# Kernel optimization log

Hardware: AMD Instinct MI355X
Metric: run time of the kernel (lower is better)

## Reference

```python
import jax, jax.numpy as jnp
import numpy as np

H, E, V = 1024, 8, 32000
B, S = 2, 2048
RANK, ALPHA = 4, 1.0
LORA_SCALE = ALPHA / RANK
TOP_K = 2
C1, DEC = 4096, 256
CACHE_SIZES = np.array([C1 - i * DEC for i in range(E)])  # [4096,...,2304]
CMAX = int(CACHE_SIZES.max())
H2 = H // 2  # pyramid compression ratio 0.5


def setup_inputs() -> dict:
    key = jax.random.key(0)
    ks = jax.random.split(key, 24)
    n = lambda k, shape, s=1.0: jax.random.normal(k, shape, dtype=jnp.float32) * s
    w = 1.0 / np.sqrt(H)
    inp = {
        "x": n(ks[0], (B, S, H)),
        "query": n(ks[1], (B, S, H)),
        "cache_values": n(ks[2], (E, CMAX, H)),
        "cache_importance": jax.random.uniform(ks[3], (E, CMAX), dtype=jnp.float32),
        "Wr": n(ks[4], (H, E), w),
        "Wexp": n(ks[5], (E, H, H), w),
        "bexp": jnp.zeros((E, H), jnp.float32),
        "Aexp": n(ks[6], (E, H, RANK), w),
        "Bexp": n(ks[7], (E, RANK, H), w),
        "Wq": n(ks[8], (H, H), w),
        "bq": jnp.zeros((H,), jnp.float32),
        "Wk": n(ks[9], (H, H), w),
        "bk": jnp.zeros((H,), jnp.float32),
        "Aq": n(ks[10], (H, RANK), w),
        "Bq": n(ks[11], (RANK, H), w),
        "Ak": n(ks[12], (H, RANK), w),
        "Bk": n(ks[13], (RANK, H), w),
        "Wd": n(ks[14], (H, H2), w),
        "Wu": n(ks[15], (H2, H), 1.0 / np.sqrt(H2)),
        "Av": n(ks[16], (E, H, RANK), w),
        "Bv": n(ks[17], (E, RANK, H), w),
        "Wv": n(ks[18], (H, V), w),
        "bv": jnp.zeros((V,), jnp.float32),
    }
    # compressor weights are per-expert in the original (one per KVCache)
    inp["Wd"] = n(ks[19], (E, H, H2), w)
    inp["Wu"] = n(ks[20], (E, H2, H), 1.0 / np.sqrt(H2))
    return inp


def reference(x, query, cache_values, cache_importance, Wr, Wexp, bexp, Aexp, Bexp,
              Wq, bq, Wk, bk, Aq, Bq, Ak, Bk, Wd, Wu, Av, Bv, Wv, bv):
    # ---- AdaptiveRouter: softmax gate, top-2, renormalize, scatter to dense ----
    gate = jax.nn.softmax(jnp.einsum("bsh,he->bse", x, Wr), axis=-1)       # [B,S,E]
    topv, topi = jax.lax.top_k(gate, TOP_K)                                 # [B,S,K]
    topv = topv / jnp.sum(topv, axis=-1, keepdims=True)
    rw = jnp.sum(jax.nn.one_hot(topi, E, dtype=x.dtype) * topv[..., None], axis=-2)  # [B,S,E]

    # ---- compute_token_importance: LoRA-augmented q/k projections + attention ----
    q = query @ Wq + bq + LORA_SCALE * ((query @ Aq) @ Bq)                  # [B,S,H]
    k = x @ Wk + bk + LORA_SCALE * ((x @ Ak) @ Bk)                          # [B,S,H]
    att = jax.nn.softmax(jnp.einsum("bqh,bkh->bqk", q, k) / np.sqrt(H), axis=-1)
    importance = jnp.sum(att, axis=1)                                       # [B,S] (sum over queries)

    # ---- per-expert KV cache: pyramid compress (down-gelu-up, importance gate) + value LoRA, masked mean ----
    valid = jnp.asarray(np.arange(CMAX)[None, :] < CACHE_SIZES[:, None], x.dtype)  # [E,Cmax]
    h = jax.nn.gelu(jnp.einsum("ech,ehd->ecd", cache_values, Wd))           # [E,Cmax,H2]
    comp = jnp.einsum("ecd,edh->ech", h, Wu) * jax.nn.sigmoid(cache_importance)[..., None]
    comp = comp + LORA_SCALE * jnp.einsum("ech,ehr,erd->ecd", comp, Av, Bv)
    cached = jnp.sum(comp * valid[..., None], axis=1) / jnp.asarray(CACHE_SIZES, x.dtype)[:, None]  # [E,H]

    # ---- dense loop over all LoRA experts (original runs every expert on every token) ----
    eo = jnp.einsum("bsh,ehd->bsed", x, Wexp) + bexp                        # [B,S,E,H]
    eo = eo + LORA_SCALE * jnp.einsum("bsh,ehr,erd->bsed", x, Aexp, Bexp)
    eo = eo + cached[None, None]                                            # broadcast cached values
    expert_output = jnp.einsum("bsed,bse->bsd", eo, rw)                     # routed combine

    logits = expert_output @ Wv + bv                                        # [B,S,V]
    return logits, importance
```

## Files before the change

### kernel.cpp

```cpp
#include <hip/hip_runtime.h>

typedef __bf16 bf16_t;
typedef __bf16 bf16x4 __attribute__((ext_vector_type(4)));
typedef __bf16 bf16x8 __attribute__((ext_vector_type(8)));
typedef float f32x4 __attribute__((ext_vector_type(4)));

#define AS1 __attribute__((address_space(1)))
#define AS3 __attribute__((address_space(3)))
#define BAR() asm volatile("s_barrier" ::: "memory")

__device__ __forceinline__ void gload_lds16(const void* g, void* l) {
  __builtin_amdgcn_global_load_lds((AS1 void*)g, (AS3 void*)l, 16, 0, 0);
}

__device__ __forceinline__ void stage_tile(const bf16_t* g, int ld, bf16_t* lds, int tid) {
  int w = tid >> 6, lane = tid & 63;
#pragma unroll
  for (int r = 0; r < 2; ++r) {
    int rowbase = r * 64 + w * 16;
    const bf16_t* gp = g + (long)(rowbase + (lane >> 2)) * ld + (lane & 3) * 8;
    bf16_t* lp = lds + rowbase * 32;
    gload_lds16(gp, lp);
  }
}

__device__ __forceinline__ void gemm_core(const bf16_t* A, const bf16_t* Bt, int lda, int ldb,
                                          int K, int rowBase, int colBase,
                                          bf16_t* As, bf16_t* Bs, f32x4 acc[4][4]) {
  int tid = threadIdx.x;
  int lane = tid & 63, w = tid >> 6;
  int wr = w >> 1, wc = w & 1;
  int lr = lane & 15, kg = lane >> 4;
  const bf16_t* Ab = A + (long)rowBase * lda;
  const bf16_t* Bb = Bt + (long)colBase * ldb;
  for (int kt = 0; kt < K; kt += 32) {
    __syncthreads();
    stage_tile(Ab + kt, lda, As, tid);
    stage_tile(Bb + kt, ldb, Bs, tid);
    __syncthreads();
    bf16x8 a[4], b[4];
#pragma unroll
    for (int m = 0; m < 4; ++m)
      a[m] = *(const bf16x8*)&As[(wr * 64 + m * 16 + lr) * 32 + kg * 8];
#pragma unroll
    for (int n = 0; n < 4; ++n)
      b[n] = *(const bf16x8*)&Bs[(wc * 64 + n * 16 + lr) * 32 + kg * 8];
#pragma unroll
    for (int m = 0; m < 4; ++m)
#pragma unroll
      for (int n = 0; n < 4; ++n)
        acc[m][n] = __builtin_amdgcn_mfma_f32_16x16x32_bf16(a[m], b[n], acc[m][n], 0, 0, 0);
  }
}

__device__ __forceinline__ void zero_acc(f32x4 acc[4][4]) {
#pragma unroll
  for (int m = 0; m < 4; ++m)
#pragma unroll
    for (int n = 0; n < 4; ++n)
#pragma unroll
      for (int i = 0; i < 4; ++i) acc[m][n][i] = 0.f;
}

__global__ __launch_bounds__(256) void k_cast(const float* in, bf16_t* out, long n4) {
  long i = (long)blockIdx.x * 256 + threadIdx.x;
  if (i >= n4) return;
  float4 v = ((const float4*)in)[i];
  bf16_t* o = out + i * 4;
  o[0] = (bf16_t)v.x; o[1] = (bf16_t)v.y; o[2] = (bf16_t)v.z; o[3] = (bf16_t)v.w;
}

__global__ __launch_bounds__(256) void k_prep_wt(const float* W, const float* A, const float* Bm,
                                                 bf16_t* out, int K, int N,
                                                 long wstride, long astride, long bstride, long ostride) {
  __shared__ float tile[64][65];
  int e = blockIdx.z;
  W += (long)e * wstride;
  out += (long)e * ostride;
  if (A) { A += (long)e * astride; Bm += (long)e * bstride; }
  int k0 = blockIdx.x * 64, n0 = blockIdx.y * 64;
  int tid = threadIdx.x;
  int tn = tid & 63, tk = tid >> 6;
#pragma unroll 4
  for (int i = 0; i < 16; ++i) {
    int k = tk + i * 4;
    float v = W[(long)(k0 + k) * N + (n0 + tn)];
    if (A) {
      const float* Ak = A + (long)(k0 + k) * 4;
      const float* Bn = Bm + n0 + tn;
      v += 0.25f * (Ak[0] * Bn[0] + Ak[1] * Bn[(long)N] + Ak[2] * Bn[2L * N] + Ak[3] * Bn[3L * N]);
    }
    tile[k][tn] = v;
  }
  __syncthreads();
#pragma unroll 4
  for (int i = 0; i < 16; ++i) {
    int n = tk + i * 4;
    out[(long)(n0 + n) * K + (k0 + tn)] = (bf16_t)tile[tn][n];
  }
}

__global__ __launch_bounds__(256) void k_router(const float* x, const float* Wr, float* rw) {
  int w = threadIdx.x >> 6, lane = threadIdx.x & 63;
  long tok = (long)blockIdx.x * 4 + w;
  const float* xr = x + tok * 1024;
  float acc[8] = {0.f, 0.f, 0.f, 0.f, 0.f, 0.f, 0.f, 0.f};
  for (int h = lane; h < 1024; h += 64) {
    float xv = xr[h];
    const float* wr8 = Wr + h * 8;
#pragma unroll
    for (int e = 0; e < 8; ++e) acc[e] += xv * wr8[e];
  }
#pragma unroll
  for (int o = 32; o; o >>= 1)
#pragma unroll
    for (int e = 0; e < 8; ++e) acc[e] += __shfl_xor(acc[e], o);
  if (lane == 0) {
    int i1 = 0;
    for (int e = 1; e < 8; ++e) if (acc[e] > acc[i1]) i1 = e;
    int i2 = (i1 == 0) ? 1 : 0;
    for (int e = 0; e < 8; ++e) { if (e == i1) continue; if (acc[e] > acc[i2]) i2 = e; }
    float g2 = expf(acc[i2] - acc[i1]);
    float d = 1.f / (1.f + g2);
    float* dst = rw + tok * 8;
#pragma unroll
    for (int e = 0; e < 8; ++e) dst[e] = (e == i1) ? d : ((e == i2) ? g2 * d : 0.f);
  }
}

__global__ __launch_bounds__(256) void k_gemm_bias_bf16(const bf16_t* A, const bf16_t* Bt,
                                                        const float* bias, bf16_t* out,
                                                        int K, int lda, int ldb, int ldc) {
  __shared__ bf16_t As[4096] __attribute__((aligned(16)));
  __shared__ bf16_t Bs[4096] __attribute__((aligned(16)));
  int rowBase = blockIdx.x * 128, colBase = blockIdx.y * 128;
  f32x4 acc[4][4];
  zero_acc(acc);
  gemm_core(A, Bt, lda, ldb, K, rowBase, colBase, As, Bs, acc);
  int tid = threadIdx.x, lane = tid & 63, w = tid >> 6;
  int wr = w >> 1, wc = w & 1, lc = lane & 15, kg = lane >> 4;
#pragma unroll
  for (int m = 0; m < 4; ++m)
#pragma unroll
    for (int n = 0; n < 4; ++n)
#pragma unroll
      for (int r = 0; r < 4; ++r) {
        int gr = rowBase + wr * 64 + m * 16 + kg * 4 + r;
        int gc = colBase + wc * 64 + n * 16 + lc;
        out[(long)gr * ldc + gc] = (bf16_t)(acc[m][n][r] + bias[gc]);
      }
}

template <bool NT>
__global__ __launch_bounds__(256) void k_gemm128(
    const bf16_t* __restrict__ A, long Az, const bf16_t* __restrict__ Bt, long Bz,
    const float* __restrict__ bias, float* __restrict__ out, long Oz,
    int mB, int N, int K, float scale) {
  __shared__ bf16_t As[4096] __attribute__((aligned(16)));
  __shared__ bf16_t Bs[4096] __attribute__((aligned(16)));
  __shared__ float fl[32 * 132];
  int tid = threadIdx.x;
  A += (long)blockIdx.y * Az;
  Bt += (long)blockIdx.y * Bz;
  out += (long)blockIdx.y * Oz;
  int per = gridDim.x >> 3;
  int bid = blockIdx.x;
  int swz = (bid & 7) * per + (bid >> 3);
  int rowB = swz % mB, colB = swz / mB;
  int rowBase = rowB << 7, colBase = colB << 7;
  f32x4 acc[4][4];
  zero_acc(acc);
  gemm_core(A, Bt, K, K, K, rowBase, colBase, As, Bs, acc);
  int lane = tid & 63, w = tid >> 6;
  int wr = w >> 1, wc = w & 1, lc = lane & 15, kg = lane >> 4;
  int colq = (tid & 31) * 4;
  f32x4 bb = {0.f, 0.f, 0.f, 0.f};
  if (bias) bb = *(const f32x4*)(bias + colBase + colq);
#pragma unroll
  for (int c = 0; c < 4; ++c) {
    __syncthreads();
    if (wr == (c >> 1)) {
      int m0 = (c & 1) * 2;
#pragma unroll
      for (int mm = 0; mm < 2; ++mm)
#pragma unroll
        for (int n = 0; n < 4; ++n)
#pragma unroll
          for (int r = 0; r < 4; ++r)
            fl[(mm * 16 + kg * 4 + r) * 132 + wc * 64 + n * 16 + lc] = acc[m0 + mm][n][r] * scale;
    }
    __syncthreads();
    long grow = rowBase + c * 32;
#pragma unroll
    for (int q = 0; q < 4; ++q) {
      int idx = q * 256 + tid;
      int row = idx >> 5;
      f32x4 v = *(const f32x4*)&fl[row * 132 + colq];
      v += bb;
      float* op = out + (grow + row) * (long)N + colBase + colq;
      if (NT) __builtin_nontemporal_store(v, (f32x4*)op);
      else *(f32x4*)op = v;
    }
  }
}

template <bool NT>
__global__ __launch_bounds__(512, 2) void k_gemm256(
    const bf16_t* __restrict__ A, long Az, const bf16_t* __restrict__ Bt, long Bz,
    const float* __restrict__ bias, float* __restrict__ out, long Oz,
    int mBlocks, int N, int K, int ntk, float scale) {
  __shared__ bf16_t lds[81920] __attribute__((aligned(16)));
  int tid = threadIdx.x;
  int lane = tid & 63, w = tid >> 6;
  int wr = w >> 2, wc = w & 3;
  int lr = lane & 15, kg = lane >> 4;
  A += (long)blockIdx.y * Az;
  Bt += (long)blockIdx.y * Bz;
  out += (long)blockIdx.y * Oz;

  int per = gridDim.x >> 3;
  int bid = blockIdx.x;
  int swz = (bid & 7) * per + (bid >> 3);
  int rowB = swz % mBlocks, colB = swz / mBlocks;
  long rowBase = (long)rowB << 8, colBase = (long)colB << 8;

  int colE = ((lane & 7) ^ (lane >> 3)) * 8;
  int r0 = w * 16 + (lane >> 3);
  const bf16_t* Ag = A + rowBase * K;
  const bf16_t* Bg = Bt + colBase * K;

  auto stageA = [&](int t, int h) {
    const bf16_t* g = Ag + (long)(h * 128 + r0) * K + t * 64 + colE;
    bf16_t* l = lds + (t & 1) * 16384 + h * 8192 + w * 1024;
    gload_lds16(g, l);
    gload_lds16(g + (long)8 * K, l + 512);
  };
  auto stageB = [&](int t, int h) {
    const bf16_t* g = Bg + (long)(h * 128 + r0) * K + t * 64 + colE;
    bf16_t* l = lds + 32768 + (t % 3) * 16384 + h * 8192 + w * 1024;
    gload_lds16(g, l);
    gload_lds16(g + (long)8 * K, l + 512);
  };

  f32x4 acc[8][4];
#pragma unroll
  for (int m = 0; m < 8; ++m)
#pragma unroll
    for (int n = 0; n < 4; ++n)
#pragma unroll
      for (int i = 0; i < 4; ++i) acc[m][n][i] = 0.f;

  stageB(0, 0); stageB(0, 1); stageA(0, 0); stageA(0, 1);
  if (ntk > 1) { stageB(1, 0); stageB(1, 1); }
  if (ntk > 1) asm volatile("s_waitcnt vmcnt(4)" ::: "memory");
  else         asm volatile("s_waitcnt vmcnt(0)" ::: "memory");
  BAR();

  for (int t = 0; t < ntk; ++t) {
    const bf16_t* Ar = lds + (t & 1) * 16384 + wr * 8192;
    const bf16_t* Br = lds + 32768 + (t % 3) * 16384 + (wc >> 1) * 8192;
    int bRowOff = (wc & 1) * 64;
    bf16x8 bfr[4][2];
#pragma unroll
    for (int p = 0; p < 4; ++p) {
      if (p == 0) {
#pragma unroll
        for (int n = 0; n < 4; ++n) {
          int R = bRowOff + n * 16 + lr;
#pragma unroll
          for (int ks = 0; ks < 2; ++ks)
            bfr[n][ks] = *(const bf16x8*)(Br + R * 64 + ((ks * 4 + kg) ^ (R & 7)) * 8);
        }
      }
      bf16x8 afr[2][2];
#pragma unroll
      for (int mm = 0; mm < 2; ++mm) {
        int R = p * 32 + mm * 16 + lr;
#pragma unroll
        for (int ks = 0; ks < 2; ++ks)
          afr[mm][ks] = *(const bf16x8*)(Ar + R * 64 + ((ks * 4 + kg) ^ (R & 7)) * 8);
      }
      if (p < 2) { if (t + 1 < ntk) stageA(t + 1, p); }
      else       { if (t + 2 < ntk) stageB(t + 2, p - 2); }
      BAR();
      asm volatile("s_waitcnt lgkmcnt(0)" ::: "memory");
      __builtin_amdgcn_sched_barrier(0);
      __builtin_amdgcn_s_setprio(1);
#pragma unroll
      for (int mm = 0; mm < 2; ++mm)
#pragma unroll
        for (int n = 0; n < 4; ++n)
#pragma unroll
          for (int ks = 0; ks < 2; ++ks)
            acc[p * 2 + mm][n] =
                __builtin_amdgcn_mfma_f32_16x16x32_bf16(afr[mm][ks], bfr[n][ks],
                                                        acc[p * 2 + mm][n], 0, 0, 0);
      __builtin_amdgcn_s_setprio(0);
      if (p == 3) {
        if (t + 2 < ntk)      asm volatile("s_waitcnt vmcnt(4)" ::: "memory");
        else if (t + 1 < ntk) asm volatile("s_waitcnt vmcnt(0)" ::: "memory");
      }
      BAR();
    }
  }

  float* fl = (float*)lds;
  f32x4 bb4 = {0.f, 0.f, 0.f, 0.f};
  if (bias) bb4 = ((const f32x4*)(bias + colBase))[lane];
#pragma unroll
  for (int c = 0; c < 4; ++c) {
    if ((c >> 1) == wr) {
      int mg0 = (c & 1) * 4;
#pragma unroll
      for (int j = 0; j < 4; ++j)
#pragma unroll
        for (int n = 0; n < 4; ++n) {
          int col = wc * 64 + n * 16 + lr;
          int lrow = j * 16 + kg * 4;
#pragma unroll
          for (int rr = 0; rr < 4; ++rr)
            fl[(lrow + rr) * 260 + col] = acc[mg0 + j][n][rr] * scale;
        }
    }
    BAR();
    long grow = rowBase + c * 64;
#pragma unroll
    for (int q = 0; q < 8; ++q) {
      int r = w * 8 + q;
      f32x4 v = *(const f32x4*)&fl[r * 260 + lane * 4];
      v += bb4;
      float* op = out + (grow + r) * (long)N + colBase + lane * 4;
      if (NT) __builtin_nontemporal_store(v, (f32x4*)op);
      else *(f32x4*)op = v;
    }
    BAR();
  }
}

__global__ __launch_bounds__(256) void k_expert_y(const bf16_t* x_bf, const bf16_t* wexp_t,
                                                  bf16_t* Y) {
  __shared__ bf16_t As[4096] __attribute__((aligned(16)));
  __shared__ bf16_t Bs[4096] __attribute__((aligned(16)));
  int e = blockIdx.z;
  int rowBase = blockIdx.x * 128, colBase = blockIdx.y * 128;
  f32x4 acc[4][4];
  zero_acc(acc);
  gemm_core(x_bf, wexp_t + (long)e * 1048576, 1024, 1024, 1024, rowBase, colBase, As, Bs, acc);
  bf16_t* o = Y + (long)e * 4194304;
  int tid = threadIdx.x, lane = tid & 63, w = tid >> 6;
  int wr = w >> 1, wc = w & 1, lc = lane & 15, kg = lane >> 4;
#pragma unroll
  for (int m = 0; m < 4; ++m)
#pragma unroll
    for (int n = 0; n < 4; ++n)
#pragma unroll
      for (int r = 0; r < 4; ++r) {
        int gr = rowBase + wr * 64 + m * 16 + kg * 4 + r;
        int gc = colBase + wc * 64 + n * 16 + lc;
        o[(long)gr * 1024 + gc] = (bf16_t)acc[m][n][r];
      }
}

__global__ __launch_bounds__(256) void k_combine(const bf16_t* Y, const float* rw,
                                                 const float* cbc, bf16_t* out) {
  long t = blockIdx.x;
  const float* rwt = rw + t * 8;
  int e1 = -1, e2 = -1;
  float w1 = 0.f, w2 = 0.f;
#pragma unroll
  for (int e = 0; e < 8; ++e) {
    float v = rwt[e];
    if (v > 0.f) { if (e1 < 0) { e1 = e; w1 = v; } else { e2 = e; w2 = v; } }
  }
  if (e1 < 0) { e1 = 0; }
  if (e2 < 0) { e2 = e1; w2 = 0.f; }
  const bf16_t* y1 = Y + ((long)e1 * 4096 + t) * 1024;
  const bf16_t* y2 = Y + ((long)e2 * 4096 + t) * 1024;
  const float* c1 = cbc + e1 * 1024;
  const float* c2 = cbc + e2 * 1024;
  bf16_t* o = out + t * 1024;
  int d = threadIdx.x * 4;
  bf16x4 a = *(const bf16x4*)(y1 + d);
  bf16x4 b = *(const bf16x4*)(y2 + d);
  f32x4 c1v = *(const f32x4*)(c1 + d);
  f32x4 c2v = *(const f32x4*)(c2 + d);
  bf16x4 r;
#pragma unroll
  for (int i = 0; i < 4; ++i)
    r[i] = (bf16_t)(w1 * ((float)a[i] + c1v[i]) + w2 * ((float)b[i] + c2v[i]));
  *(bf16x4*)(o + d) = r;
}

__global__ __launch_bounds__(256) void k_cache_gemm(const bf16_t* cache_bf, const bf16_t* wd_t,
                                                    const float* ci, float* partial) {
  __shared__ bf16_t As[4096] __attribute__((aligned(16)));
  __shared__ bf16_t Bs[4096] __attribute__((aligned(16)));
  __shared__ float colsum[128];
  int e = blockIdx.z;
  int rowBase = blockIdx.x * 128, colBase = blockIdx.y * 128;
  int tid = threadIdx.x;
  if (tid < 128) colsum[tid] = 0.f;
  f32x4 acc[4][4];
  zero_acc(acc);
  gemm_core(cache_bf + (long)e * 4096 * 1024, wd_t + (long)e * 512 * 1024, 1024, 1024, 1024,
            rowBase, colBase, As, Bs, acc);
  int lane = tid & 63, w = tid >> 6;
  int wr = w >> 1, wc = w & 1, lc = lane & 15, kg = lane >> 4;
  int csize = 4096 - 256 * e;
  const float* cie = ci + (long)e * 4096;
  float wf[4][4];
#pragma unroll
  for (int m = 0; m < 4; ++m)
#pragma unroll
    for (int r = 0; r < 4; ++r) {
      int c = rowBase + wr * 64 + m * 16 + kg * 4 + r;
      wf[m][r] = (c < csize) ? 1.f / (1.f + expf(-cie[c])) : 0.f;
    }
  __syncthreads();
#pragma unroll
  for (int n = 0; n < 4; ++n) {
    float s = 0.f;
#pragma unroll
    for (int m = 0; m < 4; ++m)
#pragma unroll
      for (int r = 0; r < 4; ++r) {
        float xv = acc[m][n][r];
        float t = xv + 0.044715f * xv * xv * xv;
        float gl = 0.5f * xv * (1.f + tanhf(0.7978845608028654f * t));
        s += gl * wf[m][r];
      }
    s += __shfl_xor(s, 16);
    s += __shfl_xor(s, 32);
    if (kg == 0) atomicAdd(&colsum[wc * 64 + n * 16 + lc], s);
  }
  __syncthreads();
  if (tid < 128)
    partial[((long)e * 32 + blockIdx.x) * 512 + colBase + tid] = colsum[tid];
}

__global__ __launch_bounds__(256) void k_reduce_g(const float* partial, float* g) {
  int e = blockIdx.x, tid = threadIdx.x;
  for (int j = tid; j < 512; j += 256) {
    float s = 0.f;
    for (int mx = 0; mx < 32; ++mx) s += partial[((long)e * 32 + mx) * 512 + j];
    g[e * 512 + j] = s;
  }
}

__global__ __launch_bounds__(256) void k_wu_mv(const float* g, const float* Wu, float* pre) {
  int e = blockIdx.x;
  int d = blockIdx.y * 256 + threadIdx.x;
  __shared__ float gs[512];
  for (int j = threadIdx.x; j < 512; j += 256) gs[j] = g[e * 512 + j];
  __syncthreads();
  const float* W = Wu + (long)e * 524288 + d;
  float s = 0.f;
  for (int j = 0; j < 512; ++j) s += gs[j] * W[(long)j * 1024];
  pre[e * 1024 + d] = s;
}

__global__ __launch_bounds__(256) void k_cached_fin(const float* pre, const float* Av,
                                                    const float* Bv, const float* bexp,
                                                    float* cbc) {
  int e = blockIdx.x, tid = threadIdx.x;
  __shared__ float ps[1024];
  __shared__ float tt[4];
  for (int d = tid; d < 1024; d += 256) ps[d] = pre[e * 1024 + d];
  __syncthreads();
  int w = tid >> 6, lane = tid & 63;
  {
    float s = 0.f;
    const float* Ave = Av + e * 4096;
    for (int d = lane; d < 1024; d += 64) s += ps[d] * Ave[d * 4 + w];
#pragma unroll
    for (int o = 32; o; o >>= 1) s += __shfl_xor(s, o);
    if (lane == 0) tt[w] = s;
  }
  __syncthreads();
  float inv = 1.f / (float)(4096 - 256 * e);
  const float* Bve = Bv + e * 4096;
  for (int d = tid; d < 1024; d += 256) {
    float lora = tt[0] * Bve[d] + tt[1] * Bve[1024 + d] + tt[2] * Bve[2048 + d] + tt[3] * Bve[3072 + d];
    cbc[e * 1024 + d] = (ps[d] + 0.25f * lora) * inv + bexp[e * 1024 + d];
  }
}

__global__ __launch_bounds__(256) void k_rowstat(const float* S, float* mrow, float* zinv) {
  long row = blockIdx.x;
  const float* r = S + row * 2048;
  int tid = threadIdx.x;
  float m = -3.4e38f;
  for (int c = tid; c < 2048; c += 256) m = fmaxf(m, r[c]);
#pragma unroll
  for (int o = 32; o; o >>= 1) m = fmaxf(m, __shfl_xor(m, o));
  __shared__ float sm[4], ss[4];
  if ((tid & 63) == 0) sm[tid >> 6] = m;
  __syncthreads();
  m = fmaxf(fmaxf(sm[0], sm[1]), fmaxf(sm[2], sm[3]));
  float s = 0.f;
  for (int c = tid; c < 2048; c += 256) s += expf(r[c] - m);
#pragma unroll
  for (int o = 32; o; o >>= 1) s += __shfl_xor(s, o);
  if ((tid & 63) == 0) ss[tid >> 6] = s;
  __syncthreads();
  if (tid == 0) { mrow[row] = m; zinv[row] = 1.f / (ss[0] + ss[1] + ss[2] + ss[3]); }
}

__global__ __launch_bounds__(256) void k_imp_part(const float* S, const float* mrow, const float* zinv,
                                                  float* ipart) {
  int k = blockIdx.x * 256 + threadIdx.x;
  int qc = blockIdx.y, b = blockIdx.z;
  const float* Sb = S + (long)b * 4194304;
  const float* mb = mrow + b * 2048;
  const float* zb = zinv + b * 2048;
  float s = 0.f;
  int q0 = qc * 128;
  for (int q = q0; q < q0 + 128; ++q)
    s += expf(Sb[(long)q * 2048 + k] - mb[q]) * zb[q];
  ipart[((long)b * 16 + qc) * 2048 + k] = s;
}

__global__ __launch_bounds__(256) void k_imp_fin(const float* ipart, float* out) {
  int k = blockIdx.x * 256 + threadIdx.x;
  int b = blockIdx.y;
  float s = 0.f;
  for (int qc = 0; qc < 16; ++qc) s += ipart[((long)b * 16 + qc) * 2048 + k];
  out[b * 2048 + k] = s;
}

extern "C" void kernel_launch(void* const* d_in, const int* in_sizes, int n_in,
                              void* d_out, int out_size, void* d_ws, size_t ws_size,
                              hipStream_t stream) {
  (void)in_sizes; (void)n_in; (void)out_size; (void)ws_size;
  const float* x    = (const float*)d_in[0];
  const float* query= (const float*)d_in[1];
  const float* cach = (const float*)d_in[2];
  const float* ci   = (const float*)d_in[3];
  const float* Wr   = (const float*)d_in[4];
  const float* Wexp = (const float*)d_in[5];
  const float* bexp = (const float*)d_in[6];
  const float* Aexp = (const float*)d_in[7];
  const float* Bexp = (const float*)d_in[8];
  const float* Wq   = (const float*)d_in[9];
  const float* bq   = (const float*)d_in[10];
  const float* Wk   = (const float*)d_in[11];
  const float* bk   = (const float*)d_in[12];
  const float* Aq   = (const float*)d_in[13];
  const float* Bq   = (const float*)d_in[14];
  const float* Ak   = (const float*)d_in[15];
  const float* Bk   = (const float*)d_in[16];
  const float* Wd   = (const float*)d_in[17];
  const float* Wu   = (const float*)d_in[18];
  const float* Av   = (const float*)d_in[19];
  const float* Bv   = (const float*)d_in[20];
  const float* Wv   = (const float*)d_in[21];
  const float* bv   = (const float*)d_in[22];
  float* out = (float*)d_out;

  size_t off = 0;
  char* base = (char*)d_ws;
  auto carve = [&](size_t bytes) { char* p = base + off; off = (off + bytes + 255) & ~(size_t)255; return (void*)p; };
  bf16_t* x_bf     = (bf16_t*)carve(8388608);
  bf16_t* query_bf = (bf16_t*)carve(8388608);
  bf16_t* q_bf     = (bf16_t*)carve(8388608);
  bf16_t* k_bf     = (bf16_t*)carve(8388608);
  bf16_t* expert_bf= (bf16_t*)carve(8388608);
  bf16_t* wq_t     = (bf16_t*)carve(2097152);
  bf16_t* wk_t     = (bf16_t*)carve(2097152);
  bf16_t* wd_t     = (bf16_t*)carve(8388608);
  bf16_t* wexp_t   = (bf16_t*)carve(16777216);
  float*  s_att    = (float*)carve(33554432);
  float*  mrow     = (float*)carve(16384);
  float*  zinv     = (float*)carve(16384);
  float*  rw       = (float*)carve(131072);
  float*  partial  = (float*)carve(524288);
  float*  gbuf     = (float*)carve(16384);
  float*  pre      = (float*)carve(32768);
  float*  cbc      = (float*)carve(32768);
  float*  ipart    = (float*)carve(262144);
  void*   uni      = carve(71303168);
  bf16_t* cache_bf = (bf16_t*)uni;
  bf16_t* Y        = (bf16_t*)uni;
  bf16_t* wv_t     = (bf16_t*)uni;

  k_cast<<<4096, 256, 0, stream>>>(x, x_bf, 1048576);
  k_cast<<<4096, 256, 0, stream>>>(query, query_bf, 1048576);
  k_cast<<<32768, 256, 0, stream>>>(cach, cache_bf, 8388608);
  k_prep_wt<<<dim3(16, 16, 1), 256, 0, stream>>>(Wq, Aq, Bq, wq_t, 1024, 1024, 0, 0, 0, 0);
  k_prep_wt<<<dim3(16, 16, 1), 256, 0, stream>>>(Wk, Ak, Bk, wk_t, 1024, 1024, 0, 0, 0, 0);
  k_prep_wt<<<dim3(16, 8, 8), 256, 0, stream>>>(Wd, nullptr, nullptr, wd_t, 1024, 512, 524288, 0, 0, 524288);
  k_prep_wt<<<dim3(16, 16, 8), 256, 0, stream>>>(Wexp, Aexp, Bexp, wexp_t, 1024, 1024, 1048576, 4096, 4096, 1048576);
  k_router<<<1024, 256, 0, stream>>>(x, Wr, rw);
  k_gemm_bias_bf16<<<dim3(32, 8), 256, 0, stream>>>(query_bf, wq_t, bq, q_bf, 1024, 1024, 1024, 1024);
  k_gemm_bias_bf16<<<dim3(32, 8), 256, 0, stream>>>(x_bf, wk_t, bk, k_bf, 1024, 1024, 1024, 1024);
  k_gemm128<false><<<dim3(256, 2), 256, 0, stream>>>(q_bf, 2097152, k_bf, 2097152, nullptr,
                                                     s_att, 4194304, 16, 2048, 1024, 0.03125f);
  k_rowstat<<<4096, 256, 0, stream>>>(s_att, mrow, zinv);
  k_imp_part<<<dim3(8, 16, 2), 256, 0, stream>>>(s_att, mrow, zinv, ipart);
  k_imp_fin<<<dim3(8, 2), 256, 0, stream>>>(ipart, out + 131072000L);
  k_cache_gemm<<<dim3(32, 4, 8), 256, 0, stream>>>(cache_bf, wd_t, ci, partial);
  k_reduce_g<<<8, 256, 0, stream>>>(partial, gbuf);
  k_wu_mv<<<dim3(8, 4), 256, 0, stream>>>(gbuf, Wu, pre);
  k_cached_fin<<<8, 256, 0, stream>>>(pre, Av, Bv, bexp, cbc);
  k_expert_y<<<dim3(32, 8, 8), 256, 0, stream>>>(x_bf, wexp_t, Y);
  k_combine<<<4096, 256, 0, stream>>>(Y, rw, cbc, expert_bf);
  k_prep_wt<<<dim3(16, 500, 1), 256, 0, stream>>>(Wv, nullptr, nullptr, wv_t, 1024, 32000, 0, 0, 0, 0);
  k_gemm256<true><<<dim3(2000, 1), 512, 0, stream>>>(expert_bf, 0, wv_t, 0, bv,
                                                     out, 0, 16, 32000, 1024, 16, 1.0f);
}
```

Baseline: 761.2 us.

## Move cache and expert GEMMs onto shared 256-tile pipelined core, batch Q/K projections

Factors the 256x256 pipelined MFMA main loop into a shared helper. The per-expert cache down-projection and the dense expert GEMM now run on it, replacing the older 128-tile kernels, with a GELU/importance column-sum epilogue and an LDS-staged bf16 store epilogue respectively. The Q and K projection GEMMs are merged into one launch via a z-dimension batch. To make the z stride valid, query_bf is placed directly before x_bf in the workspace. The aim is higher data reuse and MFMA efficiency plus fewer launches. The cost is larger LDS use per block and fewer blocks per launch, which could hurt occupancy or tail balance.

```diff
diff --git a/kernel.cpp b/kernel.cpp
--- a/kernel.cpp
+++ b/kernel.cpp
@@ -62,6 +62,84 @@
       for (int i = 0; i < 4; ++i) acc[m][n][i] = 0.f;
 }
 
+__device__ __forceinline__ void pipe256(const bf16_t* __restrict__ Ag,
+                                        const bf16_t* __restrict__ Bg,
+                                        int K, int ntk, bf16_t* lds, f32x4 acc[8][4]) {
+  int tid = threadIdx.x;
+  int lane = tid & 63, w = tid >> 6;
+  int wr = w >> 2, wc = w & 3;
+  int lr = lane & 15, kg = lane >> 4;
+  int colE = ((lane & 7) ^ (lane >> 3)) * 8;
+  int r0 = w * 16 + (lane >> 3);
+
+  auto stageA = [&](int t, int h) {
+    const bf16_t* g = Ag + (long)(h * 128 + r0) * K + t * 64 + colE;
+    bf16_t* l = lds + (t & 1) * 16384 + h * 8192 + w * 1024;
+    gload_lds16(g, l);
+    gload_lds16(g + (long)8 * K, l + 512);
+  };
+  auto stageB = [&](int t, int h) {
+    const bf16_t* g = Bg + (long)(h * 128 + r0) * K + t * 64 + colE;
+    bf16_t* l = lds + 32768 + (t % 3) * 16384 + h * 8192 + w * 1024;
+    gload_lds16(g, l);
+    gload_lds16(g + (long)8 * K, l + 512);
+  };
+
+  stageB(0, 0); stageB(0, 1); stageA(0, 0); stageA(0, 1);
+  if (ntk > 1) { stageB(1, 0); stageB(1, 1); }
+  if (ntk > 1) asm volatile("s_waitcnt vmcnt(4)" ::: "memory");
+  else         asm volatile("s_waitcnt vmcnt(0)" ::: "memory");
+  BAR();
+
+  for (int t = 0; t < ntk; ++t) {
+    const bf16_t* Ar = lds + (t & 1) * 16384 + wr * 8192;
+    const bf16_t* Br = lds + 32768 + (t % 3) * 16384 + (wc >> 1) * 8192;
+    int bRowOff = (wc & 1) * 64;
+    bf16x8 bfr[4][2];
+#pragma unroll
+    for (int p = 0; p < 4; ++p) {
+      if (p == 0) {
+#pragma unroll
+        for (int n = 0; n < 4; ++n) {
+          int R = bRowOff + n * 16 + lr;
+#pragma unroll
+          for (int ks = 0; ks < 2; ++ks)
+            bfr[n][ks] = *(const bf16x8*)(Br + R * 64 + ((ks * 4 + kg) ^ (R & 7)) * 8);
+        }
+      }
+      bf16x8 afr[2][2];
+#pragma unroll
+      for (int mm = 0; mm < 2; ++mm) {
+        int R = p * 32 + mm * 16 + lr;
+#pragma unroll
+        for (int ks = 0; ks < 2; ++ks)
+          afr[mm][ks] = *(const bf16x8*)(Ar + R * 64 + ((ks * 4 + kg) ^ (R & 7)) * 8);
+      }
+      if (p < 2) { if (t + 1 < ntk) stageA(t + 1, p); }
+      else       { if (t + 2 < ntk) stageB(t + 2, p - 2); }
+      BAR();
+      asm volatile("s_waitcnt lgkmcnt(0)" ::: "memory");
+      __builtin_amdgcn_sched_barrier(0);
+      __builtin_amdgcn_s_setprio(1);
+#pragma unroll
+      for (int mm = 0; mm < 2; ++mm)
+#pragma unroll
+        for (int n = 0; n < 4; ++n)
+#pragma unroll
+          for (int ks = 0; ks < 2; ++ks)
+            acc[p * 2 + mm][n] =
+                __builtin_amdgcn_mfma_f32_16x16x32_bf16(afr[mm][ks], bfr[n][ks],
+                                                        acc[p * 2 + mm][n], 0, 0, 0);
+      __builtin_amdgcn_s_setprio(0);
+      if (p == 3) {
+        if (t + 2 < ntk)      asm volatile("s_waitcnt vmcnt(4)" ::: "memory");
+        else if (t + 1 < ntk) asm volatile("s_waitcnt vmcnt(0)" ::: "memory");
+      }
+      BAR();
+    }
+  }
+}
+
 __global__ __launch_bounds__(256) void k_cast(const float* in, bf16_t* out, long n4) {
   long i = (long)blockIdx.x * 256 + threadIdx.x;
   if (i >= n4) return;
@@ -128,15 +206,19 @@
   }
 }
 
-__global__ __launch_bounds__(256) void k_gemm_bias_bf16(const bf16_t* A, const bf16_t* Bt,
-                                                        const float* bias, bf16_t* out,
-                                                        int K, int lda, int ldb, int ldc) {
+__global__ __launch_bounds__(256) void k_gemm_bias_bf16(const bf16_t* A, long Az,
+                                                        const bf16_t* Bt, long Bz,
+                                                        const float* bias0, const float* bias1,
+                                                        bf16_t* out, long Oz, int K, int ldc) {
   __shared__ bf16_t As[4096] __attribute__((aligned(16)));
   __shared__ bf16_t Bs[4096] __attribute__((aligned(16)));
+  int z = blockIdx.z;
+  A += (long)z * Az; Bt += (long)z * Bz; out += (long)z * Oz;
+  const float* bias = z ? bias1 : bias0;
   int rowBase = blockIdx.x * 128, colBase = blockIdx.y * 128;
   f32x4 acc[4][4];
   zero_acc(acc);
-  gemm_core(A, Bt, lda, ldb, K, rowBase, colBase, As, Bs, acc);
+  gemm_core(A, Bt, K, K, K, rowBase, colBase, As, Bs, acc);
   int tid = threadIdx.x, lane = tid & 63, w = tid >> 6;
   int wr = w >> 1, wc = w & 1, lc = lane & 15, kg = lane >> 4;
 #pragma unroll
@@ -217,31 +299,12 @@
   A += (long)blockIdx.y * Az;
   Bt += (long)blockIdx.y * Bz;
   out += (long)blockIdx.y * Oz;
-
   int per = gridDim.x >> 3;
   int bid = blockIdx.x;
   int swz = (bid & 7) * per + (bid >> 3);
   int rowB = swz % mBlocks, colB = swz / mBlocks;
   long rowBase = (long)rowB << 8, colBase = (long)colB << 8;
 
-  int colE = ((lane & 7) ^ (lane >> 3)) * 8;
-  int r0 = w * 16 + (lane >> 3);
-  const bf16_t* Ag = A + rowBase * K;
-  const bf16_t* Bg = Bt + colBase * K;
-
-  auto stageA = [&](int t, int h) {
-    const bf16_t* g = Ag + (long)(h * 128 + r0) * K + t * 64 + colE;
-    bf16_t* l = lds + (t & 1) * 16384 + h * 8192 + w * 1024;
-    gload_lds16(g, l);
-    gload_lds16(g + (long)8 * K, l + 512);
-  };
-  auto stageB = [&](int t, int h) {
-    const bf16_t* g = Bg + (long)(h * 128 + r0) * K + t * 64 + colE;
-    bf16_t* l = lds + 32768 + (t % 3) * 16384 + h * 8192 + w * 1024;
-    gload_lds16(g, l);
-    gload_lds16(g + (long)8 * K, l + 512);
-  };
-
   f32x4 acc[8][4];
 #pragma unroll
   for (int m = 0; m < 8; ++m)
@@ -249,60 +312,7 @@
     for (int n = 0; n < 4; ++n)
 #pragma unroll
       for (int i = 0; i < 4; ++i) acc[m][n][i] = 0.f;
-
-  stageB(0, 0); stageB(0, 1); stageA(0, 0); stageA(0, 1);
-  if (ntk > 1) { stageB(1, 0); stageB(1, 1); }
-  if (ntk > 1) asm volatile("s_waitcnt vmcnt(4)" ::: "memory");
-  else         asm volatile("s_waitcnt vmcnt(0)" ::: "memory");
-  BAR();
-
-  for (int t = 0; t < ntk; ++t) {
-    const bf16_t* Ar = lds + (t & 1) * 16384 + wr * 8192;
-    const bf16_t* Br = lds + 32768 + (t % 3) * 16384 + (wc >> 1) * 8192;
-    int bRowOff = (wc & 1) * 64;
-    bf16x8 bfr[4][2];
-#pragma unroll
-    for (int p = 0; p < 4; ++p) {
-      if (p == 0) {
-#pragma unroll
-        for (int n = 0; n < 4; ++n) {
-          int R = bRowOff + n * 16 + lr;
-#pragma unroll
-          for (int ks = 0; ks < 2; ++ks)
-            bfr[n][ks] = *(const bf16x8*)(Br + R * 64 + ((ks * 4 + kg) ^ (R & 7)) * 8);
-        }
-      }
-      bf16x8 afr[2][2];
-#pragma unroll
-      for (int mm = 0; mm < 2; ++mm) {
-        int R = p * 32 + mm * 16 + lr;
-#pragma unroll
-        for (int ks = 0; ks < 2; ++ks)
-          afr[mm][ks] = *(const bf16x8*)(Ar + R * 64 + ((ks * 4 + kg) ^ (R & 7)) * 8);
-      }
-      if (p < 2) { if (t + 1 < ntk) stageA(t + 1, p); }
-      else       { if (t + 2 < ntk) stageB(t + 2, p - 2); }
-      BAR();
-      asm volatile("s_waitcnt lgkmcnt(0)" ::: "memory");
-      __builtin_amdgcn_sched_barrier(0);
-      __builtin_amdgcn_s_setprio(1);
-#pragma unroll
-      for (int mm = 0; mm < 2; ++mm)
-#pragma unroll
-        for (int n = 0; n < 4; ++n)
-#pragma unroll
-          for (int ks = 0; ks < 2; ++ks)
-            acc[p * 2 + mm][n] =
-                __builtin_amdgcn_mfma_f32_16x16x32_bf16(afr[mm][ks], bfr[n][ks],
-                                                        acc[p * 2 + mm][n], 0, 0, 0);
-      __builtin_amdgcn_s_setprio(0);
-      if (p == 3) {
-        if (t + 2 < ntk)      asm volatile("s_waitcnt vmcnt(4)" ::: "memory");
-        else if (t + 1 < ntk) asm volatile("s_waitcnt vmcnt(0)" ::: "memory");
-      }
-      BAR();
-    }
-  }
+  pipe256(A + rowBase * K, Bt + colBase * K, K, ntk, lds, acc);
 
   float* fl = (float*)lds;
   f32x4 bb4 = {0.f, 0.f, 0.f, 0.f};
@@ -337,28 +347,115 @@
   }
 }
 
-__global__ __launch_bounds__(256) void k_expert_y(const bf16_t* x_bf, const bf16_t* wexp_t,
-                                                  bf16_t* Y) {
-  __shared__ bf16_t As[4096] __attribute__((aligned(16)));
-  __shared__ bf16_t Bs[4096] __attribute__((aligned(16)));
-  int e = blockIdx.z;
-  int rowBase = blockIdx.x * 128, colBase = blockIdx.y * 128;
-  f32x4 acc[4][4];
-  zero_acc(acc);
-  gemm_core(x_bf, wexp_t + (long)e * 1048576, 1024, 1024, 1024, rowBase, colBase, As, Bs, acc);
-  bf16_t* o = Y + (long)e * 4194304;
-  int tid = threadIdx.x, lane = tid & 63, w = tid >> 6;
-  int wr = w >> 1, wc = w & 1, lc = lane & 15, kg = lane >> 4;
-#pragma unroll
-  for (int m = 0; m < 4; ++m)
+__global__ __launch_bounds__(512, 2) void k_gemm256h(
+    const bf16_t* __restrict__ A, long Az, const bf16_t* __restrict__ Bt, long Bz,
+    bf16_t* __restrict__ out, long Oz, int mBlocks, int N, int K, int ntk) {
+  __shared__ bf16_t lds[81920] __attribute__((aligned(16)));
+  int tid = threadIdx.x;
+  int lane = tid & 63, w = tid >> 6;
+  int wr = w >> 2, wc = w & 3;
+  int lr = lane & 15, kg = lane >> 4;
+  A += (long)blockIdx.y * Az;
+  Bt += (long)blockIdx.y * Bz;
+  out += (long)blockIdx.y * Oz;
+  int per = gridDim.x >> 3;
+  int bid = blockIdx.x;
+  int swz = (bid & 7) * per + (bid >> 3);
+  int rowB = swz % mBlocks, colB = swz / mBlocks;
+  long rowBase = (long)rowB << 8, colBase = (long)colB << 8;
+
+  f32x4 acc[8][4];
+#pragma unroll
+  for (int m = 0; m < 8; ++m)
 #pragma unroll
     for (int n = 0; n < 4; ++n)
 #pragma unroll
-      for (int r = 0; r < 4; ++r) {
-        int gr = rowBase + wr * 64 + m * 16 + kg * 4 + r;
-        int gc = colBase + wc * 64 + n * 16 + lc;
-        o[(long)gr * 1024 + gc] = (bf16_t)acc[m][n][r];
+      for (int i = 0; i < 4; ++i) acc[m][n][i] = 0.f;
+  pipe256(A + rowBase * K, Bt + colBase * K, K, ntk, lds, acc);
+
+  float* fl = (float*)lds;
+#pragma unroll
+  for (int c = 0; c < 4; ++c) {
+    if ((c >> 1) == wr) {
+      int mg0 = (c & 1) * 4;
+#pragma unroll
+      for (int j = 0; j < 4; ++j)
+#pragma unroll
+        for (int n = 0; n < 4; ++n) {
+          int col = wc * 64 + n * 16 + lr;
+          int lrow = j * 16 + kg * 4;
+#pragma unroll
+          for (int rr = 0; rr < 4; ++rr)
+            fl[(lrow + rr) * 260 + col] = acc[mg0 + j][n][rr];
+        }
+    }
+    BAR();
+    long grow = rowBase + c * 64;
+#pragma unroll
+    for (int q = 0; q < 8; ++q) {
+      int r = w * 8 + q;
+      f32x4 v = *(const f32x4*)&fl[r * 260 + lane * 4];
+      bf16x4 h;
+#pragma unroll
+      for (int i = 0; i < 4; ++i) h[i] = (bf16_t)v[i];
+      *(bf16x4*)(out + (grow + r) * (long)N + colBase + lane * 4) = h;
+    }
+    BAR();
+  }
+}
+
+__global__ __launch_bounds__(512, 2) void k_cache256(
+    const bf16_t* __restrict__ cache_bf, const bf16_t* __restrict__ wd_t,
+    const float* __restrict__ ci, float* __restrict__ partial) {
+  __shared__ bf16_t lds[81920] __attribute__((aligned(16)));
+  int tid = threadIdx.x;
+  int lane = tid & 63, w = tid >> 6;
+  int wr = w >> 2, wc = w & 3;
+  int lr = lane & 15, kg = lane >> 4;
+  int e = blockIdx.y;
+  const bf16_t* A = cache_bf + (long)e * 4194304;
+  const bf16_t* Bt = wd_t + (long)e * 524288;
+  int per = gridDim.x >> 3;
+  int bid = blockIdx.x;
+  int swz = (bid & 7) * per + (bid >> 3);
+  int rowB = swz % 16, colB = swz / 16;
+  long rowBase = (long)rowB << 8, colBase = (long)colB << 8;
+
+  f32x4 acc[8][4];
+#pragma unroll
+  for (int m = 0; m < 8; ++m)
+#pragma unroll
+    for (int n = 0; n < 4; ++n)
+#pragma unroll
+      for (int i = 0; i < 4; ++i) acc[m][n][i] = 0.f;
+  pipe256(A + rowBase * 1024, Bt + colBase * 1024, 1024, 16, lds, acc);
+
+  float* colsum = (float*)lds;
+  if (tid < 256) colsum[tid] = 0.f;
+  __syncthreads();
+  int csize = 4096 - 256 * e;
+  const float* cie = ci + (long)e * 4096;
+  float s[4] = {0.f, 0.f, 0.f, 0.f};
+#pragma unroll
+  for (int mg = 0; mg < 8; ++mg)
+#pragma unroll
+    for (int rr = 0; rr < 4; ++rr) {
+      int row = (int)rowBase + wr * 128 + mg * 16 + kg * 4 + rr;
+      float wf = (row < csize) ? 1.f / (1.f + expf(-cie[row])) : 0.f;
+#pragma unroll
+      for (int n = 0; n < 4; ++n) {
+        float xv = acc[mg][n][rr];
+        float t = xv + 0.044715f * xv * xv * xv;
+        float gl = 0.5f * xv * (1.f + tanhf(0.7978845608028654f * t));
+        s[n] += gl * wf;
       }
+    }
+#pragma unroll
+  for (int n = 0; n < 4; ++n)
+    atomicAdd(&colsum[wc * 64 + n * 16 + lr], s[n]);
+  __syncthreads();
+  if (tid < 256)
+    partial[((long)e * 16 + rowB) * 512 + colB * 256 + tid] = colsum[tid];
 }
 
 __global__ __launch_bounds__(256) void k_combine(const bf16_t* Y, const float* rw,
@@ -391,58 +488,11 @@
   *(bf16x4*)(o + d) = r;
 }
 
-__global__ __launch_bounds__(256) void k_cache_gemm(const bf16_t* cache_bf, const bf16_t* wd_t,
-                                                    const float* ci, float* partial) {
-  __shared__ bf16_t As[4096] __attribute__((aligned(16)));
-  __shared__ bf16_t Bs[4096] __attribute__((aligned(16)));
-  __shared__ float colsum[128];
-  int e = blockIdx.z;
-  int rowBase = blockIdx.x * 128, colBase = blockIdx.y * 128;
-  int tid = threadIdx.x;
-  if (tid < 128) colsum[tid] = 0.f;
-  f32x4 acc[4][4];
-  zero_acc(acc);
-  gemm_core(cache_bf + (long)e * 4096 * 1024, wd_t + (long)e * 512 * 1024, 1024, 1024, 1024,
-            rowBase, colBase, As, Bs, acc);
-  int lane = tid & 63, w = tid >> 6;
-  int wr = w >> 1, wc = w & 1, lc = lane & 15, kg = lane >> 4;
-  int csize = 4096 - 256 * e;
-  const float* cie = ci + (long)e * 4096;
-  float wf[4][4];
-#pragma unroll
-  for (int m = 0; m < 4; ++m)
-#pragma unroll
-    for (int r = 0; r < 4; ++r) {
-      int c = rowBase + wr * 64 + m * 16 + kg * 4 + r;
-      wf[m][r] = (c < csize) ? 1.f / (1.f + expf(-cie[c])) : 0.f;
-    }
-  __syncthreads();
-#pragma unroll
-  for (int n = 0; n < 4; ++n) {
-    float s = 0.f;
-#pragma unroll
-    for (int m = 0; m < 4; ++m)
-#pragma unroll
-      for (int r = 0; r < 4; ++r) {
-        float xv = acc[m][n][r];
-        float t = xv + 0.044715f * xv * xv * xv;
-        float gl = 0.5f * xv * (1.f + tanhf(0.7978845608028654f * t));
-        s += gl * wf[m][r];
-      }
-    s += __shfl_xor(s, 16);
-    s += __shfl_xor(s, 32);
-    if (kg == 0) atomicAdd(&colsum[wc * 64 + n * 16 + lc], s);
-  }
-  __syncthreads();
-  if (tid < 128)
-    partial[((long)e * 32 + blockIdx.x) * 512 + colBase + tid] = colsum[tid];
-}
-
 __global__ __launch_bounds__(256) void k_reduce_g(const float* partial, float* g) {
   int e = blockIdx.x, tid = threadIdx.x;
   for (int j = tid; j < 512; j += 256) {
     float s = 0.f;
-    for (int mx = 0; mx < 32; ++mx) s += partial[((long)e * 32 + mx) * 512 + j];
+    for (int mx = 0; mx < 16; ++mx) s += partial[((long)e * 16 + mx) * 512 + j];
     g[e * 512 + j] = s;
   }
 }
@@ -560,8 +610,8 @@
   size_t off = 0;
   char* base = (char*)d_ws;
   auto carve = [&](size_t bytes) { char* p = base + off; off = (off + bytes + 255) & ~(size_t)255; return (void*)p; };
+  bf16_t* query_bf = (bf16_t*)carve(8388608);
   bf16_t* x_bf     = (bf16_t*)carve(8388608);
-  bf16_t* query_bf = (bf16_t*)carve(8388608);
   bf16_t* q_bf     = (bf16_t*)carve(8388608);
   bf16_t* k_bf     = (bf16_t*)carve(8388608);
   bf16_t* expert_bf= (bf16_t*)carve(8388608);
@@ -573,7 +623,7 @@
   float*  mrow     = (float*)carve(16384);
   float*  zinv     = (float*)carve(16384);
   float*  rw       = (float*)carve(131072);
-  float*  partial  = (float*)carve(524288);
+  float*  partial  = (float*)carve(262144);
   float*  gbuf     = (float*)carve(16384);
   float*  pre      = (float*)carve(32768);
   float*  cbc      = (float*)carve(32768);
@@ -591,18 +641,19 @@
   k_prep_wt<<<dim3(16, 8, 8), 256, 0, stream>>>(Wd, nullptr, nullptr, wd_t, 1024, 512, 524288, 0, 0, 524288);
   k_prep_wt<<<dim3(16, 16, 8), 256, 0, stream>>>(Wexp, Aexp, Bexp, wexp_t, 1024, 1024, 1048576, 4096, 4096, 1048576);
   k_router<<<1024, 256, 0, stream>>>(x, Wr, rw);
-  k_gemm_bias_bf16<<<dim3(32, 8), 256, 0, stream>>>(query_bf, wq_t, bq, q_bf, 1024, 1024, 1024, 1024);
-  k_gemm_bias_bf16<<<dim3(32, 8), 256, 0, stream>>>(x_bf, wk_t, bk, k_bf, 1024, 1024, 1024, 1024);
+  k_gemm_bias_bf16<<<dim3(32, 8, 2), 256, 0, stream>>>(query_bf, 4194304, wq_t, 1048576,
+                                                       bq, bk, q_bf, 4194304, 1024, 1024);
   k_gemm128<false><<<dim3(256, 2), 256, 0, stream>>>(q_bf, 2097152, k_bf, 2097152, nullptr,
                                                      s_att, 4194304, 16, 2048, 1024, 0.03125f);
   k_rowstat<<<4096, 256, 0, stream>>>(s_att, mrow, zinv);
   k_imp_part<<<dim3(8, 16, 2), 256, 0, stream>>>(s_att, mrow, zinv, ipart);
   k_imp_fin<<<dim3(8, 2), 256, 0, stream>>>(ipart, out + 131072000L);
-  k_cache_gemm<<<dim3(32, 4, 8), 256, 0, stream>>>(cache_bf, wd_t, ci, partial);
+  k_cache256<<<dim3(32, 8), 512, 0, stream>>>(cache_bf, wd_t, ci, partial);
   k_reduce_g<<<8, 256, 0, stream>>>(partial, gbuf);
   k_wu_mv<<<dim3(8, 4), 256, 0, stream>>>(gbuf, Wu, pre);
   k_cached_fin<<<8, 256, 0, stream>>>(pre, Av, Bv, bexp, cbc);
-  k_expert_y<<<dim3(32, 8, 8), 256, 0, stream>>>(x_bf, wexp_t, Y);
+  k_gemm256h<<<dim3(64, 8), 512, 0, stream>>>(x_bf, 0, wexp_t, 1048576, Y, 4194304,
+                                              16, 1024, 1024, 16);
   k_combine<<<4096, 256, 0, stream>>>(Y, rw, cbc, expert_bf);
   k_prep_wt<<<dim3(16, 500, 1), 256, 0, stream>>>(Wv, nullptr, nullptr, wv_t, 1024, 32000, 0, 0, 0, 0);
   k_gemm256<true><<<dim3(2000, 1), 512, 0, stream>>>(expert_bf, 0, wv_t, 0, bv,
```

New measurement: 761.8 us. About the same (+0.1%).
